# Optimization experiments

Hardware: AMD Instinct MI355X
Metric: run time of the kernel (lower is better)

The kernel has to match this reference:

```python
import jax, jax.numpy as jnp
import numpy as np

HEADS = 8
EPS = 1e-5


def setup_inputs() -> dict:
    key = jax.random.key(0)
    ks = jax.random.split(key, 4)
    B, S, N, C = 1, 192, 256, 256
    msa = jax.random.normal(ks[0], (B, S, N, C), dtype=jnp.float32)
    w_qkv = jax.random.normal(ks[1], (3 * C, C), dtype=jnp.float32) * 0.02
    b_qkv = jnp.zeros((3 * C,), dtype=jnp.float32)
    w_out = jax.random.normal(ks[2], (C, C), dtype=jnp.float32) * 0.02
    b_out = jnp.zeros((C,), dtype=jnp.float32)
    gamma = jnp.ones((C,), dtype=jnp.float32)
    beta = jnp.zeros((C,), dtype=jnp.float32)
    return {"msa": msa, "w_qkv": w_qkv, "b_qkv": b_qkv, "w_out": w_out,
            "b_out": b_out, "gamma": gamma, "beta": beta}


def reference(msa, w_qkv, b_qkv, w_out, b_out, gamma, beta):
    B, S, N, C = msa.shape
    H = HEADS
    D = C // H
    scale = D ** -0.5
    # column attention: attend over the S (MSA depth) axis per residue n
    msa_t = jnp.transpose(msa, (0, 2, 1, 3))                 # [B,N,S,C]
    qkv = msa_t @ w_qkv.T + b_qkv                             # [B,N,S,3C]
    qkv = qkv.reshape(B, N, S, 3, H, D)
    q, k, v = qkv[..., 0, :, :], qkv[..., 1, :, :], qkv[..., 2, :, :]  # [B,N,S,H,D]
    attn = jnp.einsum('bnshd,bnthd->bnhst', q, k) * scale     # [B,N,H,S,S]
    attn = jax.nn.softmax(attn, axis=-1)
    out = jnp.einsum('bnhst,bnthd->bnshd', attn, v).reshape(B, N, S, C)
    out = jnp.transpose(out, (0, 2, 1, 3))                    # [B,S,N,C]
    out = out @ w_out.T + b_out
    x = msa + out
    mu = jnp.mean(x, axis=-1, keepdims=True)
    var = jnp.mean(jnp.square(x - mu), axis=-1, keepdims=True)
    return (x - mu) * jax.lax.rsqrt(var + EPS) * gamma + beta
```

## Files before the change

kernel.cpp:

```cpp
#include <hip/hip_runtime.h>
#include <stdint.h>

#define S_DIM 192
#define N_DIM 256
#define C_DIM 256
#define H_DIM 8
#define D_DIM 32
#define QKV_STRIDE (N_DIM * H_DIM * S_DIM * D_DIM)

typedef float f32x4 __attribute__((ext_vector_type(4)));
typedef float f32x16 __attribute__((ext_vector_type(16)));
typedef short bf16x8 __attribute__((ext_vector_type(8)));

__device__ __forceinline__ unsigned short f2bf(float f) {
  union { float f; unsigned u; } v; v.f = f;
  unsigned r = v.u + 0x7FFFu + ((v.u >> 16) & 1u);
  return (unsigned short)(r >> 16);
}

__device__ __forceinline__ unsigned cvt_pk_bf16(float lo, float hi) {
  unsigned r;
  asm("v_cvt_pk_bf16_f32 %0, %1, %2" : "=v"(r) : "v"(lo), "v"(hi));
  return r;
}

__device__ __forceinline__ void gl2lds16(const void* g, void* l) {
  __builtin_amdgcn_global_load_lds(
      (const __attribute__((address_space(1))) unsigned int*)g,
      (__attribute__((address_space(3))) unsigned int*)l, 16, 0, 0);
}

__global__ __launch_bounds__(256) void k_prep(const float* __restrict__ msa,
                                              unsigned short* __restrict__ A,
                                              const float* __restrict__ wq,
                                              const float* __restrict__ wo,
                                              unsigned short* __restrict__ dq,
                                              unsigned short* __restrict__ do_) {
  int b = blockIdx.x;
  if (b < 12288) {
    int tid = b * 256 + threadIdx.x;
    int token = tid >> 6;
    int c4 = tid & 63;
    int n = token / S_DIM;
    int s = token - n * S_DIM;
    float4 v = *(const float4*)(msa + ((size_t)(s * N_DIM + n) << 8) + (c4 << 2));
    ushort4 o;
    o.x = f2bf(v.x); o.y = f2bf(v.y); o.z = f2bf(v.z); o.w = f2bf(v.w);
    *(ushort4*)(A + ((size_t)token << 8) + (c4 << 2)) = o;
  } else {
    int tid = (b - 12288) * 256 + threadIdx.x;
    const float* src; unsigned short* dst; int idx;
    if (tid < 49152) { src = wq; dst = dq; idx = tid; }
    else { src = wo; dst = do_; idx = tid - 49152; }
    float4 v = *(const float4*)(src + (size_t)idx * 4);
    ushort4 o;
    o.x = f2bf(v.x); o.y = f2bf(v.y); o.z = f2bf(v.z); o.w = f2bf(v.w);
    *(ushort4*)(dst + (size_t)idx * 4) = o;
  }
}

__global__ __launch_bounds__(256) void k_qkv(const unsigned short* __restrict__ A,
                                             const unsigned short* __restrict__ W,
                                             const float* __restrict__ bq,
                                             unsigned short* __restrict__ qkv) {
  __shared__ unsigned short As[128 * 64];
  __shared__ unsigned short Bs[128 * 64];
  const int tid = threadIdx.x;
  const int lane = tid & 63, wid = tid >> 6;
  const int l16 = lane & 15, lg = lane >> 4;
  const int wr = wid >> 1, wc = wid & 1;
  const int bm0 = blockIdx.x * 128;
  const int bn0 = blockIdx.y * 128;
  const int lrow = lane >> 3, lchunk = lane & 7;
  const int sw = ((lchunk ^ lrow) * 8);

  f32x4 acc[4][4] = {};

  for (int ks = 0; ks < 4; ks++) {
    const int k0 = ks * 64;
    __syncthreads();
#pragma unroll
    for (int q = 0; q < 4; q++) {
      int base_row = wid * 32 + q * 8;
      gl2lds16(A + (size_t)(bm0 + base_row + lrow) * 256 + k0 + sw, &As[base_row * 64]);
    }
#pragma unroll
    for (int q = 0; q < 4; q++) {
      int base_row = wid * 32 + q * 8;
      gl2lds16(W + (size_t)(bn0 + base_row + lrow) * 256 + k0 + sw, &Bs[base_row * 64]);
    }
    __syncthreads();
#pragma unroll
    for (int kk = 0; kk < 2; kk++) {
      const int xr = ((kk * 4 + lg) ^ (l16 & 7)) * 8;
      bf16x8 a[4], b[4];
#pragma unroll
      for (int m = 0; m < 4; m++)
        a[m] = *(const bf16x8*)&As[(wr * 64 + m * 16 + l16) * 64 + xr];
#pragma unroll
      for (int n2 = 0; n2 < 4; n2++)
        b[n2] = *(const bf16x8*)&Bs[(wc * 64 + n2 * 16 + l16) * 64 + xr];
      if (bn0 < 512) {
#pragma unroll
        for (int m = 0; m < 4; m++)
#pragma unroll
          for (int n2 = 0; n2 < 4; n2++)
            acc[m][n2] = __builtin_amdgcn_mfma_f32_16x16x32_bf16(b[n2], a[m], acc[m][n2], 0, 0, 0);
      } else {
#pragma unroll
        for (int m = 0; m < 4; m++)
#pragma unroll
          for (int n2 = 0; n2 < 4; n2++)
            acc[m][n2] = __builtin_amdgcn_mfma_f32_16x16x32_bf16(a[m], b[n2], acc[m][n2], 0, 0, 0);
      }
    }
  }

  const int t3 = bn0 >> 8;
  if (t3 < 2) {
#pragma unroll
    for (int n2 = 0; n2 < 4; n2++) {
      int j0 = bn0 + wc * 64 + n2 * 16 + lg * 4;
      float4 b4 = *(const float4*)&bq[j0];
      int c0 = j0 & 255;
      int h = c0 >> 5, d0 = c0 & 31;
#pragma unroll
      for (int m = 0; m < 4; m++) {
        int token = bm0 + wr * 64 + m * 16 + l16;
        int n = token / S_DIM;
        int s = token - n * S_DIM;
        ushort4 o;
        o.x = f2bf(acc[m][n2][0] + b4.x);
        o.y = f2bf(acc[m][n2][1] + b4.y);
        o.z = f2bf(acc[m][n2][2] + b4.z);
        o.w = f2bf(acc[m][n2][3] + b4.w);
        *(ushort4*)(qkv + (size_t)t3 * QKV_STRIDE +
                    ((size_t)((n * 8 + h) * 192 + s)) * 32 + d0) = o;
      }
    }
  } else {
#pragma unroll
    for (int n2 = 0; n2 < 4; n2++) {
      int j = bn0 + wc * 64 + n2 * 16 + l16;
      int hd = j - 512;
      int h = hd >> 5, d = hd & 31;
      float bias = bq[j];
#pragma unroll
      for (int m = 0; m < 4; m++) {
        int t0 = bm0 + wr * 64 + m * 16 + lg * 4;
        int n = t0 / S_DIM;
        int s0 = t0 - n * S_DIM;
        ushort4 o;
        o.x = f2bf(acc[m][n2][0] + bias);
        o.y = f2bf(acc[m][n2][1] + bias);
        o.z = f2bf(acc[m][n2][2] + bias);
        o.w = f2bf(acc[m][n2][3] + bias);
        *(ushort4*)(qkv + (size_t)2 * QKV_STRIDE + ((size_t)(n * 8 + h) * 32 + d) * 192 + s0) = o;
      }
    }
  }
}

__global__ __launch_bounds__(384) void k_attn2(const unsigned short* __restrict__ qkv,
                                               unsigned short* __restrict__ attn_out) {
  const int lane = threadIdx.x & 63;
  const int l32 = lane & 31;
  const int hi = lane >> 5;
  const int qt = threadIdx.x >> 6;
  const int nh = blockIdx.x;
  const int n = nh >> 3, h = nh & 7;
  const unsigned short* Qp = qkv + (size_t)nh * (192 * 32);
  const unsigned short* Kp = qkv + (size_t)QKV_STRIDE + (size_t)nh * (192 * 32);
  const unsigned short* Vt = qkv + (size_t)2 * QKV_STRIDE + (size_t)nh * (32 * 192);
  const int q0 = qt * 32;

  bf16x8 bq0 = *(const bf16x8*)(Qp + (q0 + l32) * 32 + hi * 8);
  bf16x8 bq1 = *(const bf16x8*)(Qp + (q0 + l32) * 32 + 16 + hi * 8);

  f32x16 accO = {};
  float m_run = -1e30f, l_run = 0.f;
  const float scale = 0.17677669529663687f;
  const float DEFER = 8.0f / 0.17677669529663687f;

  bf16x8 ka0 = *(const bf16x8*)(Kp + l32 * 32 + hi * 8);
  bf16x8 ka1 = *(const bf16x8*)(Kp + l32 * 32 + 16 + hi * 8);
  bf16x8 va0 = *(const bf16x8*)(Vt + (size_t)l32 * 192 + hi * 8);
  bf16x8 va1 = *(const bf16x8*)(Vt + (size_t)l32 * 192 + 16 + hi * 8);

#pragma unroll
  for (int t = 0; t < 6; t++) {
    bf16x8 kn0, kn1, vn0, vn1;
    if (t < 5) {
      kn0 = *(const bf16x8*)(Kp + ((t + 1) * 32 + l32) * 32 + hi * 8);
      kn1 = *(const bf16x8*)(Kp + ((t + 1) * 32 + l32) * 32 + 16 + hi * 8);
      vn0 = *(const bf16x8*)(Vt + (size_t)l32 * 192 + (t + 1) * 32 + hi * 8);
      vn1 = *(const bf16x8*)(Vt + (size_t)l32 * 192 + (t + 1) * 32 + 16 + hi * 8);
    }
    f32x16 sv = {};
    sv = __builtin_amdgcn_mfma_f32_32x32x16_bf16(ka0, bq0, sv, 0, 0, 0);
    sv = __builtin_amdgcn_mfma_f32_32x32x16_bf16(ka1, bq1, sv, 0, 0, 0);

    float tmx = sv[0];
#pragma unroll
    for (int r = 1; r < 16; r++) tmx = fmaxf(tmx, sv[r]);
    tmx = fmaxf(tmx, __shfl_xor(tmx, 32));

    bool need = tmx > m_run + DEFER;
    if (__ballot(need)) {
      float m_new = fmaxf(m_run, tmx);
      float corr = __expf((m_run - m_new) * scale);
      l_run *= corr;
#pragma unroll
      for (int r = 0; r < 16; r++) {
        int qr = (r & 3) + 8 * (r >> 2) + 4 * hi;
        accO[r] *= __shfl(corr, qr);
      }
      m_run = m_new;
    }

    float ssum = 0.f;
#pragma unroll
    for (int r = 0; r < 16; r++) {
      float p2 = __expf((sv[r] - m_run) * scale);
      sv[r] = p2;
      ssum += p2;
    }
    ssum += __shfl_xor(ssum, 32);
    l_run += ssum;

    unsigned pk[8];
#pragma unroll
    for (int g = 0; g < 4; g++) {
      pk[2 * g]     = cvt_pk_bf16(sv[4 * g],     sv[4 * g + 1]);
      pk[2 * g + 1] = cvt_pk_bf16(sv[4 * g + 2], sv[4 * g + 3]);
    }

#pragma unroll
    for (int kh = 0; kh < 2; kh++) {
      unsigned sa = hi ? pk[4 * kh]     : pk[4 * kh + 2];
      unsigned sb = hi ? pk[4 * kh + 1] : pk[4 * kh + 3];
      unsigned pa = __shfl_xor((int)sa, 32);
      unsigned pb = __shfl_xor((int)sb, 32);
      union { unsigned u[4]; bf16x8 v; } af;
      af.u[0] = hi ? pa : pk[4 * kh];
      af.u[1] = hi ? pb : pk[4 * kh + 1];
      af.u[2] = hi ? pk[4 * kh + 2] : pa;
      af.u[3] = hi ? pk[4 * kh + 3] : pb;
      accO = __builtin_amdgcn_mfma_f32_32x32x16_bf16(af.v, kh ? va1 : va0, accO, 0, 0, 0);
    }
    ka0 = kn0; ka1 = kn1; va0 = vn0; va1 = vn1;
  }

  float inv = 1.0f / l_run;
#pragma unroll
  for (int r = 0; r < 16; r++) {
    int qr = (r & 3) + 8 * (r >> 2) + 4 * hi;
    float v = accO[r] * __shfl(inv, qr);
    attn_out[((size_t)((q0 + qr) * 256 + n)) * 256 + h * 32 + l32] = f2bf(v);
  }
}

__global__ __launch_bounds__(256) void k_out(const unsigned short* __restrict__ Aat,
                                             const unsigned short* __restrict__ W,
                                             const float* __restrict__ bo,
                                             const float* __restrict__ msa,
                                             const float* __restrict__ gamma,
                                             const float* __restrict__ beta,
                                             float* __restrict__ out) {
  __shared__ unsigned short As[128 * 64];
  __shared__ unsigned short Bs[256 * 64];
  const int tid = threadIdx.x;
  const int lane = tid & 63, wid = tid >> 6;
  const int l16 = lane & 15, lg = lane >> 4;
  const int bm0 = blockIdx.x * 128;
  const int lrow = lane >> 3, lchunk = lane & 7;
  const int sw = ((lchunk ^ lrow) * 8);

  f32x4 acc[2][16] = {};

  for (int ks = 0; ks < 4; ks++) {
    const int k0 = ks * 64;
    __syncthreads();
#pragma unroll
    for (int q = 0; q < 4; q++) {
      int base_row = wid * 32 + q * 8;
      gl2lds16(Aat + (size_t)(bm0 + base_row + lrow) * 256 + k0 + sw, &As[base_row * 64]);
    }
#pragma unroll
    for (int q = 0; q < 8; q++) {
      int base_row = wid * 64 + q * 8;
      gl2lds16(W + (size_t)(base_row + lrow) * 256 + k0 + sw, &Bs[base_row * 64]);
    }
    __syncthreads();
#pragma unroll
    for (int kk = 0; kk < 2; kk++) {
      const int xr = ((kk * 4 + lg) ^ (l16 & 7)) * 8;
      bf16x8 a[2];
#pragma unroll
      for (int m = 0; m < 2; m++)
        a[m] = *(const bf16x8*)&As[(wid * 32 + m * 16 + l16) * 64 + xr];
#pragma unroll
      for (int c = 0; c < 16; c++) {
        bf16x8 b = *(const bf16x8*)&Bs[(c * 16 + l16) * 64 + xr];
#pragma unroll
        for (int m = 0; m < 2; m++)
          acc[m][c] = __builtin_amdgcn_mfma_f32_16x16x32_bf16(a[m], b, acc[m][c], 0, 0, 0);
      }
    }
  }

#pragma unroll
  for (int m = 0; m < 2; m++) {
#pragma unroll
    for (int c = 0; c < 16; c++) {
      int col = c * 16 + l16;
      float bias = bo[col];
#pragma unroll
      for (int i = 0; i < 4; i++) {
        int row = bm0 + wid * 32 + m * 16 + lg * 4 + i;
        acc[m][c][i] += bias + msa[(size_t)row * 256 + col];
      }
    }
#pragma unroll
    for (int i = 0; i < 4; i++) {
      float s1 = 0.f, s2 = 0.f;
#pragma unroll
      for (int c = 0; c < 16; c++) { float x = acc[m][c][i]; s1 += x; s2 += x * x; }
      s1 += __shfl_xor(s1, 1); s2 += __shfl_xor(s2, 1);
      s1 += __shfl_xor(s1, 2); s2 += __shfl_xor(s2, 2);
      s1 += __shfl_xor(s1, 4); s2 += __shfl_xor(s2, 4);
      s1 += __shfl_xor(s1, 8); s2 += __shfl_xor(s2, 8);
      float mu = s1 * (1.0f / 256.0f);
      float var = s2 * (1.0f / 256.0f) - mu * mu;
      float rstd = rsqrtf(var + 1e-5f);
      int row = bm0 + wid * 32 + m * 16 + lg * 4 + i;
#pragma unroll
      for (int c = 0; c < 16; c++) {
        int col = c * 16 + l16;
        float y = (acc[m][c][i] - mu) * rstd * gamma[col] + beta[col];
        out[(size_t)row * 256 + col] = y;
      }
    }
  }
}

extern "C" void kernel_launch(void* const* d_in, const int* in_sizes, int n_in,
                              void* d_out, int out_size, void* d_ws, size_t ws_size,
                              hipStream_t stream) {
  const float* msa   = (const float*)d_in[0];
  const float* w_qkv = (const float*)d_in[1];
  const float* b_qkv = (const float*)d_in[2];
  const float* w_out = (const float*)d_in[3];
  const float* b_out = (const float*)d_in[4];
  const float* gamma = (const float*)d_in[5];
  const float* beta  = (const float*)d_in[6];
  float* out = (float*)d_out;

  char* ws = (char*)d_ws;
  unsigned short* A      = (unsigned short*)(ws);
  unsigned short* qkvbuf = (unsigned short*)(ws + 25165824ull);
  unsigned short* wq_bf  = (unsigned short*)(ws + 4ull * 25165824ull);
  unsigned short* wo_bf  = (unsigned short*)(ws + 4ull * 25165824ull + 393216ull);

  k_prep<<<12544, 256, 0, stream>>>(msa, A, w_qkv, w_out, wq_bf, wo_bf);
  dim3 g2(384, 6);
  k_qkv<<<g2, 256, 0, stream>>>(A, wq_bf, b_qkv, qkvbuf);
  k_attn2<<<2048, 384, 0, stream>>>(qkvbuf, A);
  k_out<<<384, 256, 0, stream>>>(A, wo_bf, b_out, msa, gamma, beta, out);
}
```

Before: 126.8 us.

## Load QKV GEMM operands directly from global into registers with prefetch

Measured after the change: 173.4 us. +36.7%, slower.

```diff
diff --git a/kernel.cpp b/kernel.cpp
--- a/kernel.cpp
+++ b/kernel.cpp
@@ -59,61 +59,54 @@
   }
 }
 
-__global__ __launch_bounds__(256) void k_qkv(const unsigned short* __restrict__ A,
-                                             const unsigned short* __restrict__ W,
-                                             const float* __restrict__ bq,
-                                             unsigned short* __restrict__ qkv) {
-  __shared__ unsigned short As[128 * 64];
-  __shared__ unsigned short Bs[128 * 64];
+__global__ __launch_bounds__(256, 3) void k_qkv(const unsigned short* __restrict__ A,
+                                                const unsigned short* __restrict__ W,
+                                                const float* __restrict__ bq,
+                                                unsigned short* __restrict__ qkv) {
   const int tid = threadIdx.x;
   const int lane = tid & 63, wid = tid >> 6;
   const int l16 = lane & 15, lg = lane >> 4;
   const int wr = wid >> 1, wc = wid & 1;
-  const int bm0 = blockIdx.x * 128;
-  const int bn0 = blockIdx.y * 128;
-  const int lrow = lane >> 3, lchunk = lane & 7;
-  const int sw = ((lchunk ^ lrow) * 8);
+  const int p = blockIdx.x;
+  const int o = (p & 7) * 288 + (p >> 3);
+  const int bm0 = (o / 6) * 128;
+  const int bn0 = (o % 6) * 128;
+
+  const unsigned short* Ap = A + (size_t)(bm0 + wr * 64 + l16) * 256 + lg * 8;
+  const unsigned short* Wp = W + (size_t)(bn0 + wc * 64 + l16) * 256 + lg * 8;
 
   f32x4 acc[4][4] = {};
-
-  for (int ks = 0; ks < 4; ks++) {
-    const int k0 = ks * 64;
-    __syncthreads();
-#pragma unroll
-    for (int q = 0; q < 4; q++) {
-      int base_row = wid * 32 + q * 8;
-      gl2lds16(A + (size_t)(bm0 + base_row + lrow) * 256 + k0 + sw, &As[base_row * 64]);
-    }
-#pragma unroll
-    for (int q = 0; q < 4; q++) {
-      int base_row = wid * 32 + q * 8;
-      gl2lds16(W + (size_t)(bn0 + base_row + lrow) * 256 + k0 + sw, &Bs[base_row * 64]);
-    }
-    __syncthreads();
-#pragma unroll
-    for (int kk = 0; kk < 2; kk++) {
-      const int xr = ((kk * 4 + lg) ^ (l16 & 7)) * 8;
-      bf16x8 a[4], b[4];
+  bf16x8 a[4], b[4], an[4], bn_[4];
+
+#pragma unroll
+  for (int m = 0; m < 4; m++) a[m] = *(const bf16x8*)(Ap + m * 16 * 256);
+#pragma unroll
+  for (int n2 = 0; n2 < 4; n2++) b[n2] = *(const bf16x8*)(Wp + n2 * 16 * 256);
+
+#pragma unroll
+  for (int ks = 0; ks < 8; ks++) {
+    if (ks < 7) {
+      const int k1 = (ks + 1) * 32;
+#pragma unroll
+      for (int m = 0; m < 4; m++) an[m] = *(const bf16x8*)(Ap + m * 16 * 256 + k1);
+#pragma unroll
+      for (int n2 = 0; n2 < 4; n2++) bn_[n2] = *(const bf16x8*)(Wp + n2 * 16 * 256 + k1);
+    }
+    if (bn0 < 512) {
 #pragma unroll
       for (int m = 0; m < 4; m++)
-        a[m] = *(const bf16x8*)&As[(wr * 64 + m * 16 + l16) * 64 + xr];
-#pragma unroll
-      for (int n2 = 0; n2 < 4; n2++)
-        b[n2] = *(const bf16x8*)&Bs[(wc * 64 + n2 * 16 + l16) * 64 + xr];
-      if (bn0 < 512) {
-#pragma unroll
-        for (int m = 0; m < 4; m++)
-#pragma unroll
-          for (int n2 = 0; n2 < 4; n2++)
-            acc[m][n2] = __builtin_amdgcn_mfma_f32_16x16x32_bf16(b[n2], a[m], acc[m][n2], 0, 0, 0);
-      } else {
-#pragma unroll
-        for (int m = 0; m < 4; m++)
-#pragma unroll
-          for (int n2 = 0; n2 < 4; n2++)
-            acc[m][n2] = __builtin_amdgcn_mfma_f32_16x16x32_bf16(a[m], b[n2], acc[m][n2], 0, 0, 0);
-      }
-    }
+#pragma unroll
+        for (int n2 = 0; n2 < 4; n2++)
+          acc[m][n2] = __builtin_amdgcn_mfma_f32_16x16x32_bf16(b[n2], a[m], acc[m][n2], 0, 0, 0);
+    } else {
+#pragma unroll
+      for (int m = 0; m < 4; m++)
+#pragma unroll
+        for (int n2 = 0; n2 < 4; n2++)
+          acc[m][n2] = __builtin_amdgcn_mfma_f32_16x16x32_bf16(a[m], b[n2], acc[m][n2], 0, 0, 0);
+    }
+#pragma unroll
+    for (int m = 0; m < 4; m++) { a[m] = an[m]; b[m] = bn_[m]; }
   }
 
   const int t3 = bn0 >> 8;
@@ -129,13 +122,13 @@
         int token = bm0 + wr * 64 + m * 16 + l16;
         int n = token / S_DIM;
         int s = token - n * S_DIM;
-        ushort4 o;
-        o.x = f2bf(acc[m][n2][0] + b4.x);
-        o.y = f2bf(acc[m][n2][1] + b4.y);
-        o.z = f2bf(acc[m][n2][2] + b4.z);
-        o.w = f2bf(acc[m][n2][3] + b4.w);
+        ushort4 o2;
+        o2.x = f2bf(acc[m][n2][0] + b4.x);
+        o2.y = f2bf(acc[m][n2][1] + b4.y);
+        o2.z = f2bf(acc[m][n2][2] + b4.z);
+        o2.w = f2bf(acc[m][n2][3] + b4.w);
         *(ushort4*)(qkv + (size_t)t3 * QKV_STRIDE +
-                    ((size_t)((n * 8 + h) * 192 + s)) * 32 + d0) = o;
+                    ((size_t)((n * 8 + h) * 192 + s)) * 32 + d0) = o2;
       }
     }
   } else {
@@ -150,12 +143,12 @@
         int t0 = bm0 + wr * 64 + m * 16 + lg * 4;
         int n = t0 / S_DIM;
         int s0 = t0 - n * S_DIM;
-        ushort4 o;
-        o.x = f2bf(acc[m][n2][0] + bias);
-        o.y = f2bf(acc[m][n2][1] + bias);
-        o.z = f2bf(acc[m][n2][2] + bias);
-        o.w = f2bf(acc[m][n2][3] + bias);
-        *(ushort4*)(qkv + (size_t)2 * QKV_STRIDE + ((size_t)(n * 8 + h) * 32 + d) * 192 + s0) = o;
+        ushort4 o2;
+        o2.x = f2bf(acc[m][n2][0] + bias);
+        o2.y = f2bf(acc[m][n2][1] + bias);
+        o2.z = f2bf(acc[m][n2][2] + bias);
+        o2.w = f2bf(acc[m][n2][3] + bias);
+        *(ushort4*)(qkv + (size_t)2 * QKV_STRIDE + ((size_t)(n * 8 + h) * 32 + d) * 192 + s0) = o2;
       }
     }
   }
@@ -363,8 +356,7 @@
   unsigned short* wo_bf  = (unsigned short*)(ws + 4ull * 25165824ull + 393216ull);
 
   k_prep<<<12544, 256, 0, stream>>>(msa, A, w_qkv, w_out, wq_bf, wo_bf);
-  dim3 g2(384, 6);
-  k_qkv<<<g2, 256, 0, stream>>>(A, wq_bf, b_qkv, qkvbuf);
+  k_qkv<<<2304, 256, 0, stream>>>(A, wq_bf, b_qkv, qkvbuf);
   k_attn2<<<2048, 384, 0, stream>>>(qkvbuf, A);
   k_out<<<384, 256, 0, stream>>>(A, wo_bf, b_out, msa, gamma, beta, out);
 }
```
